# Optimization experiments

Hardware: AMD Instinct MI355X
Metric: run time of the kernel (lower is better)

Reference implementation:

```python
import jax, jax.numpy as jnp
import numpy as np

R = 64
NF = 128
NUM_RNA = 4000
NUM_DIS = 2000
N_GLOBAL = 16
N_NODE = NUM_RNA + NUM_DIS + N_GLOBAL
E = 300000
P = 500000
MLP_DIMS = [(2 * R, R), (R, R // 2), (R // 2, 32), (32, 16), (16, 8), (8, 1)]


def _xavier(k, shape):
    fan_in = shape[0]
    fan_out = shape[-1]
    lim = float(np.sqrt(6.0 / (fan_in + fan_out)))
    return jax.random.uniform(k, shape, jnp.float32, -lim, lim)


def setup_inputs() -> dict:
    key = jax.random.key(0)
    ks = jax.random.split(key, 32)
    inp = {}
    inp["x"] = jax.random.normal(ks[0], (N_NODE, NF), jnp.float32)
    inp["adj"] = jax.random.randint(ks[1], (2, E), 0, N_NODE)
    inp["coo"] = jax.random.randint(ks[2], (P, 2), 0, NUM_DIS)
    dims = [NF, R]
    for i in range(2):
        inp[f"gw{i}"] = _xavier(ks[3 + 4 * i], (dims[i], R))
        inp[f"gas{i}"] = _xavier(ks[4 + 4 * i], (R,))
        inp[f"gad{i}"] = _xavier(ks[5 + 4 * i], (R,))
        inp[f"gb{i}"] = jnp.zeros((R,), jnp.float32)
    for j, (di, do) in enumerate(MLP_DIMS, start=1):
        inp[f"w{j}"] = _xavier(ks[12 + 2 * j], (di, do))
        inp[f"b{j}"] = jnp.zeros((do,), jnp.float32)
    return inp


def _gat_layer(x, src, dst, W, a_src, a_dst, b):
    # PyG GATConv, heads=1, add_self_loops handled by caller, negative_slope=0.2
    n = x.shape[0]
    h = x @ W                                    # [n, R]
    e = jax.nn.leaky_relu((h * a_src).sum(-1)[src] + (h * a_dst).sum(-1)[dst], 0.2)
    m = jax.ops.segment_max(e, dst, num_segments=n)
    ex = jnp.exp(e - m[dst])
    denom = jax.ops.segment_sum(ex, dst, num_segments=n)
    alpha = ex / denom[dst]                      # softmax over incoming edges
    return jax.ops.segment_sum(alpha[:, None] * h[src], dst, num_segments=n) + b


def reference(x, adj, coo, gw0, gas0, gad0, gb0, gw1, gas1, gad1, gb1,
              w1, b1, w2, b2, w3, b3, w4, b4, w5, b5, w6, b6):
    n = x.shape[0]
    loop = jnp.arange(n)
    src = jnp.concatenate([adj[0], loop])        # add self loops (GATConv default)
    dst = jnp.concatenate([adj[1], loop])
    h = _gat_layer(x, src, dst, gw0, gas0, gad0, gb0)
    h = _gat_layer(h, src, dst, gw1, gas1, gad1, gb1)
    x1 = h[:NUM_RNA]
    x2 = h[NUM_RNA:NUM_RNA + NUM_DIS]
    # vectorized per-pair gather + concat (original loops in python)
    z = jnp.concatenate([x1[coo[:, 0]], x2[coo[:, 1]]], axis=1)  # [P, 2R]
    for w, b in ((w1, b1), (w2, b2), (w3, b3), (w4, b4), (w5, b5)):
        z = jax.nn.relu(z @ w + b)
    return jax.nn.sigmoid(z @ w6 + b6)           # [P, 1]
```

## Files before the change

### kernel.cpp

```cpp
#include <hip/hip_runtime.h>
#include <cstdint>

#define N_RNA 4000
#define N_DIS 2000
#define NNODE 6016
#define NFDIM 128
#define RDIM 64
#define NE 300000
#define NET (NE + NNODE)
#define NPAIR 500000
#define NTILE (NPAIR / 16)
#define MAXD 128

typedef float vf4 __attribute__((ext_vector_type(4)));
typedef _Float16 f16x8 __attribute__((ext_vector_type(8)));
typedef _Float16 f16x2 __attribute__((ext_vector_type(2)));

union FragU {
    f16x8 f;
    f16x2 h[4];
    int   u[4];
    uint4 q;
};

__device__ __forceinline__ f16x2 pkrtz(float lo, float hi) {
    auto r = __builtin_amdgcn_cvt_pkrtz(lo, hi);
    return __builtin_bit_cast(f16x2, r);
}
__device__ __forceinline__ vf4 mfma16(const FragU& a, const FragU& b, vf4 c) {
    return __builtin_amdgcn_mfma_f32_16x16x32_f16(a.f, b.f, c, 0, 0, 0);
}
__device__ __forceinline__ unsigned addrelu2(unsigned a, unsigned b) {
    f16x2 x = __builtin_bit_cast(f16x2, a) + __builtin_bit_cast(f16x2, b);
    f16x2 zz = {(_Float16)0.f, (_Float16)0.f};
    x = __builtin_elementwise_max(x, zz);
    return __builtin_bit_cast(unsigned, x);
}

__device__ __forceinline__ FragU trans16(vf4 a, int col, int g) {
    int w0, w1;
    {
        f16x2 p0 = pkrtz(a[0], a[1]);
        f16x2 p1 = pkrtz(a[2], a[3]);
        FragU tmp; tmp.h[0] = p0; tmp.h[1] = p1;
        w0 = tmp.u[0]; w1 = tmp.u[1];
    }
    int addrA = (col + 16 * ((2 * g) & 3)) * 4;
    int addrB = (col + 16 * ((2 * g + 1) & 3)) * 4;
    int j0 = __builtin_amdgcn_ds_bpermute(addrA, w0);
    int j1 = __builtin_amdgcn_ds_bpermute(addrA, w1);
    int j2 = __builtin_amdgcn_ds_bpermute(addrB, w0);
    int j3 = __builtin_amdgcn_ds_bpermute(addrB, w1);
    bool lo2 = g < 2;
    FragU B;
    B.u[0] = lo2 ? j0 : 0;
    B.u[1] = lo2 ? j1 : 0;
    B.u[2] = lo2 ? j2 : 0;
    B.u[3] = lo2 ? j3 : 0;
    return B;
}

__global__ void setup_kernel(int* __restrict__ cur,
                             const float* __restrict__ w2, const float* __restrict__ w3,
                             const float* __restrict__ w4, const float* __restrict__ w5,
                             uint4* __restrict__ gfrag) {
    int i = blockIdx.x * blockDim.x + threadIdx.x;
    if (i < NNODE) cur[i] = 0;
    if (blockIdx.x == 0 && threadIdx.x < 64) {
        int l = threadIdx.x;
        int rho = l & 15, g = l >> 4;
        int fbase = 8 * (rho >> 2) + (rho & 3);
        FragU F;
#pragma unroll
        for (int t = 0; t < 2; t++)
#pragma unroll
            for (int kt = 0; kt < 2; kt++) {
#pragma unroll
                for (int j = 0; j < 4; j++) {
                    int k = kt * 32 + g * 8 + 2 * j;
                    F.h[j] = pkrtz(w2[k * 32 + fbase + 4 * t],
                                   w2[(k + 1) * 32 + fbase + 4 * t]);
                }
                gfrag[(t * 2 + kt) * 64 + l] = F.q;
            }
#pragma unroll
        for (int t = 0; t < 2; t++) {
#pragma unroll
            for (int j = 0; j < 4; j++) {
                int k = g * 8 + 2 * j;
                F.h[j] = pkrtz(w3[k * 32 + fbase + 4 * t],
                               w3[(k + 1) * 32 + fbase + 4 * t]);
            }
            gfrag[(4 + t) * 64 + l] = F.q;
        }
#pragma unroll
        for (int j = 0; j < 4; j++) {
            int k = g * 8 + 2 * j;
            F.h[j] = pkrtz(w4[k * 16 + rho], w4[(k + 1) * 16 + rho]);
        }
        gfrag[6 * 64 + l] = F.q;
#pragma unroll
        for (int j = 0; j < 4; j++) {
            int k = g * 8 + 2 * j;
            if (g < 2 && rho < 8)
                F.h[j] = pkrtz(w5[k * 8 + rho], w5[(k + 1) * 8 + rho]);
            else
                F.u[j] = 0;
        }
        gfrag[7 * 64 + l] = F.q;
    }
}

__global__ void fill_slots(const int* __restrict__ adj, int* __restrict__ cur,
                           int* __restrict__ slots) {
    int k = blockIdx.x * blockDim.x + threadIdx.x;
    if (k >= NET) return;
    int src, dst;
    if (k < NE) { src = adj[k]; dst = adj[NE + k]; }
    else        { src = k - NE; dst = k - NE; }
    int pos = atomicAdd(&cur[dst], 1);
    if (pos < MAXD) slots[dst * MAXD + pos] = src;
}

template <int NF>
__global__ __launch_bounds__(64) void proj_kernel(const float* __restrict__ x,
                                                  const float* __restrict__ W,
                                                  const float* __restrict__ a_s,
                                                  const float* __restrict__ a_d,
                                                  float* __restrict__ h,
                                                  float* __restrict__ ssrc,
                                                  float* __restrict__ sdst) {
    __shared__ float xr[4][NF];
    int nb = blockIdx.x * 4;
    int t = threadIdx.x;
    for (int idx = t; idx < 4 * NF; idx += 64)
        xr[idx / NF][idx % NF] = x[(size_t)nb * NF + idx];
    __syncthreads();
    float a0 = 0.f, a1 = 0.f, a2 = 0.f, a3 = 0.f;
#pragma unroll 8
    for (int k = 0; k < NF; k++) {
        float wv = W[k * RDIM + t];
        a0 = fmaf(xr[0][k], wv, a0);
        a1 = fmaf(xr[1][k], wv, a1);
        a2 = fmaf(xr[2][k], wv, a2);
        a3 = fmaf(xr[3][k], wv, a3);
    }
    h[(size_t)(nb + 0) * RDIM + t] = a0;
    h[(size_t)(nb + 1) * RDIM + t] = a1;
    h[(size_t)(nb + 2) * RDIM + t] = a2;
    h[(size_t)(nb + 3) * RDIM + t] = a3;
    float asv = a_s[t], adv = a_d[t];
    float acc[4] = {a0, a1, a2, a3};
#pragma unroll
    for (int i = 0; i < 4; i++) {
        float vs = acc[i] * asv;
        float vd = acc[i] * adv;
#pragma unroll
        for (int off = 32; off; off >>= 1) {
            vs += __shfl_down(vs, off);
            vd += __shfl_down(vd, off);
        }
        if (t == 0) { ssrc[nb + i] = vs; sdst[nb + i] = vd; }
    }
}

#define AGG_BODY_128(H, SS, SD, BIAS)                                       \
    int deg = cur[node]; if (deg > MAXD) deg = MAXD;                        \
    int beg = node * MAXD, end = beg + deg;                                 \
    float sd = (SD)[node];                                                  \
    int gg = tid >> 3, q8 = tid & 7;                                        \
    float4 A0 = {0.f, 0.f, 0.f, 0.f}, A1 = {0.f, 0.f, 0.f, 0.f};            \
    float den = 0.f;                                                        \
    for (int i = beg + gg; i < end; i += 16) {                              \
        int s = slots[i];                                                   \
        float v = (SS)[s] + sd;                                             \
        v = v > 0.f ? v : 0.2f * v;                                         \
        float ex = __expf(v);                                               \
        den += ex;                                                          \
        const float4* hp = (const float4*)((H) + (size_t)s * 64 + q8 * 8);  \
        float4 h0 = hp[0], h1 = hp[1];                                      \
        A0.x = fmaf(ex, h0.x, A0.x); A0.y = fmaf(ex, h0.y, A0.y);           \
        A0.z = fmaf(ex, h0.z, A0.z); A0.w = fmaf(ex, h0.w, A0.w);           \
        A1.x = fmaf(ex, h1.x, A1.x); A1.y = fmaf(ex, h1.y, A1.y);           \
        A1.z = fmaf(ex, h1.z, A1.z); A1.w = fmaf(ex, h1.w, A1.w);           \
    }                                                                       \
    _Pragma("unroll")                                                       \
    for (int off = 8; off <= 32; off <<= 1) {                               \
        A0.x += __shfl_xor(A0.x, off); A0.y += __shfl_xor(A0.y, off);       \
        A0.z += __shfl_xor(A0.z, off); A0.w += __shfl_xor(A0.w, off);       \
        A1.x += __shfl_xor(A1.x, off); A1.y += __shfl_xor(A1.y, off);       \
        A1.z += __shfl_xor(A1.z, off); A1.w += __shfl_xor(A1.w, off);       \
        den += __shfl_xor(den, off);                                        \
    }                                                                       \
    if (t < 8) {                                                            \
        smA[wv][8 * t + 0] = A0.x; smA[wv][8 * t + 1] = A0.y;               \
        smA[wv][8 * t + 2] = A0.z; smA[wv][8 * t + 3] = A0.w;               \
        smA[wv][8 * t + 4] = A1.x; smA[wv][8 * t + 5] = A1.y;               \
        smA[wv][8 * t + 6] = A1.z; smA[wv][8 * t + 7] = A1.w;               \
        if (t == 0) smD[wv] = den;                                          \
    }                                                                       \
    __syncthreads();                                                        \
    if (wv == 0) {                                                          \
        float inv = 1.f / (smD[0] + smD[1]);                                \
        smf[t] = (smA[0][t] + smA[1][t]) * inv + (BIAS)[t];                 \
    }

__global__ __launch_bounds__(128) void agg_proj_kernel(
    const float* __restrict__ h, const float* __restrict__ ssrc, const float* __restrict__ sdst,
    const int* __restrict__ cur, const int* __restrict__ slots,
    const float* __restrict__ bias,
    const float* __restrict__ W,
    const float* __restrict__ a_s, const float* __restrict__ a_d,
    float* __restrict__ h2, float* __restrict__ ssrc2, float* __restrict__ sdst2) {
    __shared__ float smA[2][64];
    __shared__ float smD[2];
    __shared__ float smf[64];
    int node = blockIdx.x;
    int tid = threadIdx.x;
    int wv = tid >> 6, t = tid & 63;
    AGG_BODY_128(h, ssrc, sdst, bias)
    if (wv == 0) {
        float hv = 0.f;
#pragma unroll 8
        for (int k = 0; k < 64; k++) hv = fmaf(smf[k], W[k * 64 + t], hv);
        h2[(size_t)node * 64 + t] = hv;
        float vs = hv * a_s[t];
        float vd = hv * a_d[t];
#pragma unroll
        for (int off = 32; off; off >>= 1) {
            vs += __shfl_down(vs, off);
            vd += __shfl_down(vd, off);
        }
        if (t == 0) { ssrc2[node] = vs; sdst2[node] = vd; }
    }
}

__global__ __launch_bounds__(128) void agg_pre_kernel(
    const float* __restrict__ h, const float* __restrict__ ssrc, const float* __restrict__ sdst,
    const int* __restrict__ cur, const int* __restrict__ slots,
    const float* __restrict__ bias,
    const float* __restrict__ w1, const float* __restrict__ b1,
    _Float16* __restrict__ u1h, _Float16* __restrict__ u2h) {
    __shared__ float smA[2][64];
    __shared__ float smD[2];
    __shared__ float smf[64];
    int node = blockIdx.x;
    int tid = threadIdx.x;
    int wv = tid >> 6, t = tid & 63;
    AGG_BODY_128(h, ssrc, sdst, bias)
    if (wv == 0) {
        bool rna = node < N_RNA;
        const float* w = rna ? w1 : (w1 + 64 * 64);
        float uk = rna ? b1[t] : 0.f;
#pragma unroll 8
        for (int k = 0; k < 64; k++) uk = fmaf(smf[k], w[k * 64 + t], uk);
        _Float16* dst = rna ? (u1h + (size_t)node * 64) : (u2h + (size_t)(node - N_RNA) * 64);
        dst[t] = (_Float16)uk;
    }
}

__global__ __launch_bounds__(256) void mlp_mfma_kernel(
    const _Float16* __restrict__ u1h, const _Float16* __restrict__ u2h,
    const int* __restrict__ coo, const uint4* __restrict__ gfrag,
    const float* __restrict__ b2, const float* __restrict__ b3,
    const float* __restrict__ b4, const float* __restrict__ b5,
    const float* __restrict__ w6, const float* __restrict__ b6,
    float* __restrict__ out) {
    int tid = threadIdx.x;
    const int lane = tid & 63;
    const int col  = lane & 15;
    const int g    = lane >> 4;
    const int wid  = blockIdx.x * 4 + (tid >> 6);
    const int nwaves = gridDim.x * 4;

    FragU A200, A201, A210, A211, A30, A31, A4f, A5f;
    A200.q = gfrag[0 * 64 + lane];
    A201.q = gfrag[1 * 64 + lane];
    A210.q = gfrag[2 * 64 + lane];
    A211.q = gfrag[3 * 64 + lane];
    A30.q  = gfrag[4 * 64 + lane];
    A31.q  = gfrag[5 * 64 + lane];
    A4f.q  = gfrag[6 * 64 + lane];
    A5f.q  = gfrag[7 * 64 + lane];

    float bias2[8], bias3[8], bias4[4], bias5[4], w6r[4];
#pragma unroll
    for (int i = 0; i < 8; i++) {
        bias2[i] = b2[8 * g + i];
        bias3[i] = b3[8 * g + i];
    }
#pragma unroll
    for (int r = 0; r < 4; r++) {
        bias4[r] = b4[g * 4 + r];
        bias5[r] = (g < 2) ? b5[g * 4 + r] : 0.f;
        w6r[r]   = (g < 2) ? w6[g * 4 + r] : 0.f;
    }
    float b6v = b6[0];
    const vf4 z = {0.f, 0.f, 0.f, 0.f};

    for (int tile = wid; tile < NTILE; tile += nwaves) {
        int p = tile * 16 + col;
        int2 rd = ((const int2*)coo)[p];
        const uint4* pr = (const uint4*)(u1h + (size_t)rd.x * 64);
        const uint4* pd = (const uint4*)(u2h + (size_t)rd.y * 64);
        uint4 r0 = pr[g], d0 = pd[g];
        uint4 r1 = pr[4 + g], d1 = pd[4 + g];
        FragU B0, B1;
        B0.u[0] = addrelu2(r0.x, d0.x);
        B0.u[1] = addrelu2(r0.y, d0.y);
        B0.u[2] = addrelu2(r0.z, d0.z);
        B0.u[3] = addrelu2(r0.w, d0.w);
        B1.u[0] = addrelu2(r1.x, d1.x);
        B1.u[1] = addrelu2(r1.y, d1.y);
        B1.u[2] = addrelu2(r1.z, d1.z);
        B1.u[3] = addrelu2(r1.w, d1.w);

        vf4 acc0 = mfma16(A200, B0, z);
        acc0 = mfma16(A201, B1, acc0);
        vf4 acc1 = mfma16(A210, B0, z);
        acc1 = mfma16(A211, B1, acc1);
#pragma unroll
        for (int r = 0; r < 4; r++) {
            acc0[r] = fmaxf(acc0[r] + bias2[r], 0.f);
            acc1[r] = fmaxf(acc1[r] + bias2[4 + r], 0.f);
        }
        FragU Bx;
        Bx.h[0] = pkrtz(acc0[0], acc0[1]);
        Bx.h[1] = pkrtz(acc0[2], acc0[3]);
        Bx.h[2] = pkrtz(acc1[0], acc1[1]);
        Bx.h[3] = pkrtz(acc1[2], acc1[3]);
        acc0 = mfma16(A30, Bx, z);
        acc1 = mfma16(A31, Bx, z);
#pragma unroll
        for (int r = 0; r < 4; r++) {
            acc0[r] = fmaxf(acc0[r] + bias3[r], 0.f);
            acc1[r] = fmaxf(acc1[r] + bias3[4 + r], 0.f);
        }
        Bx.h[0] = pkrtz(acc0[0], acc0[1]);
        Bx.h[1] = pkrtz(acc0[2], acc0[3]);
        Bx.h[2] = pkrtz(acc1[0], acc1[1]);
        Bx.h[3] = pkrtz(acc1[2], acc1[3]);
        vf4 a4 = mfma16(A4f, Bx, z);
#pragma unroll
        for (int r = 0; r < 4; r++) a4[r] = fmaxf(a4[r] + bias4[r], 0.f);
        Bx = trans16(a4, col, g);
        vf4 a5 = mfma16(A5f, Bx, z);
        float part = 0.f;
#pragma unroll
        for (int r = 0; r < 4; r++)
            part = fmaf(fmaxf(a5[r] + bias5[r], 0.f), w6r[r], part);
        part += __shfl_xor(part, 16);
        float sig = 1.f / (1.f + __expf(-(part + b6v)));
        if (g == 0) out[tile * 16 + col] = sig;
    }
}

extern "C" void kernel_launch(void* const* d_in, const int* in_sizes, int n_in,
                              void* d_out, int out_size, void* d_ws, size_t ws_size,
                              hipStream_t stream) {
    const float* x    = (const float*)d_in[0];
    const int*   adj  = (const int*)d_in[1];
    const int*   coo  = (const int*)d_in[2];
    const float* gw0  = (const float*)d_in[3];
    const float* gas0 = (const float*)d_in[4];
    const float* gad0 = (const float*)d_in[5];
    const float* gb0  = (const float*)d_in[6];
    const float* gw1  = (const float*)d_in[7];
    const float* gas1 = (const float*)d_in[8];
    const float* gad1 = (const float*)d_in[9];
    const float* gb1  = (const float*)d_in[10];

    char* ws = (char*)d_ws;
    size_t o = 0;
    auto take = [&](size_t bytes) -> void* {
        void* p = ws + o;
        o = (o + bytes + 255) & ~(size_t)255;
        return p;
    };
    float*     hP    = (float*)take((size_t)NNODE * RDIM * 4);
    float*     hP2   = (float*)take((size_t)NNODE * RDIM * 4);
    _Float16*  u1h   = (_Float16*)take((size_t)N_RNA * 64 * 2);
    _Float16*  u2h   = (_Float16*)take((size_t)N_DIS * 64 * 2);
    uint4*     gfrag = (uint4*)take((size_t)8 * 64 * 16);
    float*     ssrc  = (float*)take((size_t)NNODE * 4);
    float*     sdst  = (float*)take((size_t)NNODE * 4);
    float*     ssrc2 = (float*)take((size_t)NNODE * 4);
    float*     sdst2 = (float*)take((size_t)NNODE * 4);
    int*       cur   = (int*)take((size_t)NNODE * 4);
    int*       slots = (int*)take((size_t)NNODE * MAXD * 4);

    setup_kernel<<<(NNODE + 255) / 256, 256, 0, stream>>>(
        cur,
        (const float*)d_in[13], (const float*)d_in[15],
        (const float*)d_in[17], (const float*)d_in[19], gfrag);
    fill_slots<<<(NET + 255) / 256, 256, 0, stream>>>(adj, cur, slots);
    proj_kernel<NFDIM><<<NNODE / 4, 64, 0, stream>>>(x, gw0, gas0, gad0, hP, ssrc, sdst);
    agg_proj_kernel<<<NNODE, 128, 0, stream>>>(hP, ssrc, sdst, cur, slots, gb0,
                                               gw1, gas1, gad1, hP2, ssrc2, sdst2);
    agg_pre_kernel<<<N_RNA + N_DIS, 128, 0, stream>>>(
        hP2, ssrc2, sdst2, cur, slots, gb1,
        (const float*)d_in[11], (const float*)d_in[12], u1h, u2h);
    mlp_mfma_kernel<<<2048, 256, 0, stream>>>(
        u1h, u2h, coo, gfrag,
        (const float*)d_in[14], (const float*)d_in[16],
        (const float*)d_in[18], (const float*)d_in[20],
        (const float*)d_in[21], (const float*)d_in[22],
        (float*)d_out);
}
```

Baseline: 85.46 us.

## Merge slot fill with projection kernel and software-prefetch MLP tile gathers

Combines the edge-slot fill and the first-layer projection into one launch, with block ranges split by index, so the two independent jobs run concurrently and one launch is saved. Projection blocks now process 16 nodes using four waves. The MLP loop is software-pipelined: the coo indices and feature rows for the next tile load before the MFMA chain runs on the current tile, hiding gather latency at the cost of more registers. The early return in fill blocks happens before the __syncthreads that only projection blocks reach, which is uniform per block and so safe.

```diff
diff --git a/kernel.cpp b/kernel.cpp
--- a/kernel.cpp
+++ b/kernel.cpp
@@ -11,6 +11,8 @@
 #define NPAIR 500000
 #define NTILE (NPAIR / 16)
 #define MAXD 128
+#define FILLB 1196
+#define PROJB (NNODE / 16)
 
 typedef float vf4 __attribute__((ext_vector_type(4)));
 typedef _Float16 f16x8 __attribute__((ext_vector_type(8)));
@@ -111,39 +113,37 @@
     }
 }
 
-__global__ void fill_slots(const int* __restrict__ adj, int* __restrict__ cur,
-                           int* __restrict__ slots) {
-    int k = blockIdx.x * blockDim.x + threadIdx.x;
-    if (k >= NET) return;
-    int src, dst;
-    if (k < NE) { src = adj[k]; dst = adj[NE + k]; }
-    else        { src = k - NE; dst = k - NE; }
-    int pos = atomicAdd(&cur[dst], 1);
-    if (pos < MAXD) slots[dst * MAXD + pos] = src;
-}
-
-template <int NF>
-__global__ __launch_bounds__(64) void proj_kernel(const float* __restrict__ x,
-                                                  const float* __restrict__ W,
-                                                  const float* __restrict__ a_s,
-                                                  const float* __restrict__ a_d,
-                                                  float* __restrict__ h,
-                                                  float* __restrict__ ssrc,
-                                                  float* __restrict__ sdst) {
-    __shared__ float xr[4][NF];
-    int nb = blockIdx.x * 4;
-    int t = threadIdx.x;
-    for (int idx = t; idx < 4 * NF; idx += 64)
-        xr[idx / NF][idx % NF] = x[(size_t)nb * NF + idx];
+__global__ __launch_bounds__(256) void fill_proj_kernel(
+    const int* __restrict__ adj, int* __restrict__ cur, int* __restrict__ slots,
+    const float* __restrict__ x, const float* __restrict__ W,
+    const float* __restrict__ a_s, const float* __restrict__ a_d,
+    float* __restrict__ h, float* __restrict__ ssrc, float* __restrict__ sdst) {
+    int b = blockIdx.x;
+    if (b < FILLB) {
+        int k = b * 256 + threadIdx.x;
+        if (k >= NET) return;
+        int src, dst;
+        if (k < NE) { src = adj[k]; dst = adj[NE + k]; }
+        else        { src = k - NE; dst = k - NE; }
+        int pos = atomicAdd(&cur[dst], 1);
+        if (pos < MAXD) slots[dst * MAXD + pos] = src;
+        return;
+    }
+    __shared__ float xr[16][NFDIM];
+    int pb = b - FILLB;
+    int wv = threadIdx.x >> 6, t = threadIdx.x & 63;
+    int nb = pb * 16 + wv * 4;
+    for (int idx = t; idx < 4 * NFDIM; idx += 64)
+        xr[wv * 4 + idx / NFDIM][idx % NFDIM] = x[(size_t)nb * NFDIM + idx];
     __syncthreads();
     float a0 = 0.f, a1 = 0.f, a2 = 0.f, a3 = 0.f;
 #pragma unroll 8
-    for (int k = 0; k < NF; k++) {
-        float wv = W[k * RDIM + t];
-        a0 = fmaf(xr[0][k], wv, a0);
-        a1 = fmaf(xr[1][k], wv, a1);
-        a2 = fmaf(xr[2][k], wv, a2);
-        a3 = fmaf(xr[3][k], wv, a3);
+    for (int k = 0; k < NFDIM; k++) {
+        float wvv = W[k * RDIM + t];
+        a0 = fmaf(xr[wv * 4 + 0][k], wvv, a0);
+        a1 = fmaf(xr[wv * 4 + 1][k], wvv, a1);
+        a2 = fmaf(xr[wv * 4 + 2][k], wvv, a2);
+        a3 = fmaf(xr[wv * 4 + 3][k], wvv, a3);
     }
     h[(size_t)(nb + 0) * RDIM + t] = a0;
     h[(size_t)(nb + 1) * RDIM + t] = a1;
@@ -298,13 +298,7 @@
     float b6v = b6[0];
     const vf4 z = {0.f, 0.f, 0.f, 0.f};
 
-    for (int tile = wid; tile < NTILE; tile += nwaves) {
-        int p = tile * 16 + col;
-        int2 rd = ((const int2*)coo)[p];
-        const uint4* pr = (const uint4*)(u1h + (size_t)rd.x * 64);
-        const uint4* pd = (const uint4*)(u2h + (size_t)rd.y * 64);
-        uint4 r0 = pr[g], d0 = pd[g];
-        uint4 r1 = pr[4 + g], d1 = pd[4 + g];
+    auto chain = [&](uint4 r0, uint4 r1, uint4 d0, uint4 d1) -> float {
         FragU B0, B1;
         B0.u[0] = addrelu2(r0.x, d0.x);
         B0.u[1] = addrelu2(r0.y, d0.y);
@@ -314,7 +308,6 @@
         B1.u[1] = addrelu2(r1.y, d1.y);
         B1.u[2] = addrelu2(r1.z, d1.z);
         B1.u[3] = addrelu2(r1.w, d1.w);
-
         vf4 acc0 = mfma16(A200, B0, z);
         acc0 = mfma16(A201, B1, acc0);
         vf4 acc1 = mfma16(A210, B0, z);
@@ -350,8 +343,32 @@
         for (int r = 0; r < 4; r++)
             part = fmaf(fmaxf(a5[r] + bias5[r], 0.f), w6r[r], part);
         part += __shfl_xor(part, 16);
-        float sig = 1.f / (1.f + __expf(-(part + b6v)));
+        return 1.f / (1.f + __expf(-(part + b6v)));
+    };
+
+    int tile = wid;
+    uint4 r0, r1, d0, d1;
+    if (tile < NTILE) {
+        int p = tile * 16 + col;
+        int2 rd = ((const int2*)coo)[p];
+        const uint4* pr = (const uint4*)(u1h + (size_t)rd.x * 64);
+        const uint4* pd = (const uint4*)(u2h + (size_t)rd.y * 64);
+        r0 = pr[g]; r1 = pr[4 + g]; d0 = pd[g]; d1 = pd[4 + g];
+    }
+    while (tile < NTILE) {
+        int next = tile + nwaves;
+        uint4 nr0, nr1, nd0, nd1;
+        if (next < NTILE) {
+            int p = next * 16 + col;
+            int2 rd = ((const int2*)coo)[p];
+            const uint4* pr = (const uint4*)(u1h + (size_t)rd.x * 64);
+            const uint4* pd = (const uint4*)(u2h + (size_t)rd.y * 64);
+            nr0 = pr[g]; nr1 = pr[4 + g]; nd0 = pd[g]; nd1 = pd[4 + g];
+        }
+        float sig = chain(r0, r1, d0, d1);
         if (g == 0) out[tile * 16 + col] = sig;
+        tile = next;
+        r0 = nr0; r1 = nr1; d0 = nd0; d1 = nd1;
     }
 }
 
@@ -393,8 +410,8 @@
         cur,
         (const float*)d_in[13], (const float*)d_in[15],
         (const float*)d_in[17], (const float*)d_in[19], gfrag);
-    fill_slots<<<(NET + 255) / 256, 256, 0, stream>>>(adj, cur, slots);
-    proj_kernel<NFDIM><<<NNODE / 4, 64, 0, stream>>>(x, gw0, gas0, gad0, hP, ssrc, sdst);
+    fill_proj_kernel<<<FILLB + PROJB, 256, 0, stream>>>(
+        adj, cur, slots, x, gw0, gas0, gad0, hP, ssrc, sdst);
     agg_proj_kernel<<<NNODE, 128, 0, stream>>>(hP, ssrc, sdst, cur, slots, gb0,
                                                gw1, gas1, gad1, hP2, ssrc2, sdst2);
     agg_pre_kernel<<<N_RNA + N_DIS, 128, 0, stream>>>(
```

Result: faster. 82.39 us (-3.6%).
